# Kernel tuning notes

Hardware: AMD Instinct MI355X
Metric: run time of the kernel (lower is better)

Reference implementation:

```python
import jax, jax.numpy as jnp
import numpy as np

HID = 128  # args['hidden_size']


def preprocess_adj(A):
    # A: [B, N, N] -> D^{-1/2} (A + I) D^{-1/2}
    N = A.shape[1]
    A_hat = A + jnp.eye(N, dtype=A.dtype)
    d = jnp.sum(A_hat, axis=2)                     # [B, N]
    d_safe = jnp.where(d > 0, d, 1.0)
    d_inv = jnp.where(d > 0, d_safe ** -0.5, 0.0)  # inf -> 0, as in torch code
    return d_inv[:, :, None] * A_hat * d_inv[:, None, :]


def lstm(x, w_ih, w_hh, b_ih, b_hh):
    # x: [B, T, H]; PyTorch gate order i, f, g, o; zero init state
    B = x.shape[0]
    H = w_hh.shape[1]
    def step(carry, xt):
        h, c = carry
        z = xt @ w_ih.T + b_ih + h @ w_hh.T + b_hh
        i, f, g, o = jnp.split(z, 4, axis=-1)
        c = jax.nn.sigmoid(f) * c + jax.nn.sigmoid(i) * jnp.tanh(g)
        h = jax.nn.sigmoid(o) * jnp.tanh(c)
        return (h, c), h
    h0 = jnp.zeros((B, H), x.dtype)
    c0 = jnp.zeros((B, H), x.dtype)
    _, hs = jax.lax.scan(step, (h0, c0), jnp.swapaxes(x, 0, 1))
    return jnp.swapaxes(hs, 0, 1)  # [B, T, H]


def gcn_dynamic_forward(x, A_norm, conv_w, conv_b, w_ih, w_hh, b_ih, b_hh):
    # x: [B, N, HID] with N >= HID: take last HID rows as dynamic-filter input
    df_in = x[:, x.shape[1] - HID:, :]              # [B, HID, HID]
    dyn = jax.lax.conv_general_dilated(
        df_in, conv_w, window_strides=(1,), padding=[(1, 1)],
        dimension_numbers=('NCH', 'OIH', 'NCH')) + conv_b[None, :, None]
    lw = lstm(dyn, w_ih, w_hh, b_ih, b_hh)          # [B, HID, HID]
    agg = jnp.matmul(A_norm, x)                     # [B, N, HID]
    out = jax.nn.sigmoid(jnp.matmul(agg, lw))       # output activation (1-layer GCN)
    return out                                       # dropout is identity in eval


def setup_inputs() -> dict:
    key = jax.random.key(0)
    ks = jax.random.split(key, 8)
    B, N = 4, 4096
    node_embedding = jax.random.normal(ks[0], (B, N, HID), dtype=jnp.float32)
    # sparse symmetric-ish 0/1 adjacency, avg degree ~ N*0.01
    adjacency_matrix = (jax.random.uniform(ks[1], (B, N, N)) < 0.01).astype(jnp.float32)
    s = 0.05
    conv_w = jax.random.normal(ks[2], (HID, HID, 3), dtype=jnp.float32) * s
    conv_b = jax.random.normal(ks[3], (HID,), dtype=jnp.float32) * s
    w_ih = jax.random.normal(ks[4], (4 * HID, HID), dtype=jnp.float32) * s
    w_hh = jax.random.normal(ks[5], (4 * HID, HID), dtype=jnp.float32) * s
    b_ih = jax.random.normal(ks[6], (4 * HID,), dtype=jnp.float32) * s
    b_hh = jax.random.normal(ks[7], (4 * HID,), dtype=jnp.float32) * s
    return {"node_embedding": node_embedding, "adjacency_matrix": adjacency_matrix,
            "conv_w": conv_w, "conv_b": conv_b,
            "w_ih": w_ih, "w_hh": w_hh, "b_ih": b_ih, "b_hh": b_hh}


def reference(node_embedding, adjacency_matrix, conv_w, conv_b, w_ih, w_hh, b_ih, b_hh):
    A_norm = preprocess_adj(adjacency_matrix)
    return gcn_dynamic_forward(node_embedding, A_norm, conv_w, conv_b, w_ih, w_hh, b_ih, b_hh)
```

## Files before the change

kernel.cpp:

```cpp
#include <hip/hip_runtime.h>
#include <math.h>

#define N_NODES 4096
#define HIDN 128
#define MAXNZ 128

typedef float v4f __attribute__((ext_vector_type(4)));
typedef _Float16 h2 __attribute__((ext_vector_type(2)));
typedef _Float16 h8 __attribute__((ext_vector_type(8)));

__device__ __forceinline__ float fsig(float x) { return 1.0f / (1.0f + __expf(-x)); }
__device__ __forceinline__ float ftanh_(float x) { return 1.0f - 2.0f / (__expf(2.0f * x) + 1.0f); }

__global__ __launch_bounds__(512) void k_conv(
        const float* __restrict__ x, const float* __restrict__ conv_w,
        const float* __restrict__ conv_b, const float* __restrict__ w_ih,
        const float* __restrict__ b_ih, const float* __restrict__ b_hh,
        float* __restrict__ z4) {
    const int cb = blockIdx.x;
    const int b = cb >> 5;
    const int t0 = (cb & 31) * 4;
    const int tsub = threadIdx.x >> 7;
    const int h = threadIdx.x & 127;
    const int t = t0 + tsub;
    __shared__ __align__(16) float dyn_lds[4][HIDN];
    const float* xb = x + ((size_t)b * N_NODES + (N_NODES - HIDN)) * HIDN;
    const float* w = conv_w + (size_t)t * HIDN * 3;
    float a0 = conv_b[t], a1 = 0.0f, a2 = 0.0f, a3 = 0.0f;
    #pragma unroll 4
    for (int i = 0; i < HIDN; i += 4) {
        const float* xr0 = xb + (size_t)i * HIDN;
        #pragma unroll
        for (int s = 0; s < 4; ++s) {
            const float* xr = xr0 + s * HIDN;
            float w0 = w[(i + s) * 3 + 0], w1 = w[(i + s) * 3 + 1], w2 = w[(i + s) * 3 + 2];
            float left  = (h > 0)   ? xr[h - 1] : 0.0f;
            float mid   = xr[h];
            float right = (h < 127) ? xr[h + 1] : 0.0f;
            if (s == 0)      a0 += left * w0 + mid * w1 + right * w2;
            else if (s == 1) a1 += left * w0 + mid * w1 + right * w2;
            else if (s == 2) a2 += left * w0 + mid * w1 + right * w2;
            else             a3 += left * w0 + mid * w1 + right * w2;
        }
    }
    dyn_lds[tsub][h] = (a0 + a1) + (a2 + a3);
    __syncthreads();
    const float4* dyn4 = (const float4*)dyn_lds[tsub];
    const int ch = t >> 4, si = t & 15;
    for (int qg = 0; qg < 4; ++qg) {
        int u = h + 128 * qg;
        const float4* wr = (const float4*)(w_ih + (size_t)u * HIDN);
        float za = b_ih[u] + b_hh[u];
        #pragma unroll
        for (int f4 = 0; f4 < 32; ++f4) {
            float4 wv = wr[f4];
            float4 dv = dyn4[f4];
            za += wv.x * dv.x + wv.y * dv.y + wv.z * dv.z + wv.w * dv.w;
        }
        z4[(((size_t)(b * 8 + ch) * 128 + h) * 4 + qg) * 16 + si] = za;
    }
}

__global__ __launch_bounds__(256) void k_scan(
        const float* __restrict__ A, float* __restrict__ d_inv,
        int* __restrict__ cnt, int* __restrict__ idx) {
    const int wid = threadIdx.x >> 6;
    const int lane = threadIdx.x & 63;
    const int r = blockIdx.x * 4 + wid;
    const v4f* row = (const v4f*)(A + (size_t)r * N_NODES);
    int* idx_row = idx + r * MAXNZ;
    const unsigned long long below = (1ull << lane) - 1ull;
    int cbase = 0;
#define PROC1(c, col)                                                         \
    {                                                                         \
        bool nz = ((c) != 0.0f);                                              \
        unsigned long long mm = __ballot(nz);                                 \
        if (mm) {                                                             \
            if (nz) {                                                         \
                int p_ = cbase + __popcll(mm & below);                        \
                if (p_ < MAXNZ) idx_row[p_] = (col);                          \
            }                                                                 \
            cbase += __popcll(mm);                                            \
        }                                                                     \
    }
    for (int half = 0; half < 2; ++half) {
        v4f v[8];
        #pragma unroll
        for (int j = 0; j < 8; ++j)
            v[j] = row[half * 512 + j * 64 + lane];
        #pragma unroll
        for (int j = 0; j < 8; ++j) {
            int col0 = (half * 512 + j * 64 + lane) * 4;
            PROC1(v[j].x, col0 + 0);
            PROC1(v[j].y, col0 + 1);
            PROC1(v[j].z, col0 + 2);
            PROC1(v[j].w, col0 + 3);
        }
    }
#undef PROC1
    if (lane == 0) {
        cnt[r] = (cbase < MAXNZ) ? cbase : MAXNZ;
        d_inv[r] = rsqrtf((float)(cbase + 1));
    }
}

__global__ __launch_bounds__(512) void k_lstm(
        const float* __restrict__ z4, const float* __restrict__ w_hh,
        float* __restrict__ lw) {
    const int b = blockIdx.x;
    const int t = threadIdx.x;
    const int m = t >> 2;
    const int q = t & 3;
    __shared__ __align__(16) h2 hbuf[2][64];
    h2 w2[4][16];
    #pragma unroll
    for (int g = 0; g < 4; ++g) {
        const float4* wr = (const float4*)(w_hh + ((size_t)(g * HIDN + m)) * HIDN + q * 32);
        #pragma unroll
        for (int j4 = 0; j4 < 8; ++j4) {
            float4 wv = wr[j4];
            w2[g][2 * j4 + 0] = h2{(_Float16)wv.x, (_Float16)wv.y};
            w2[g][2 * j4 + 1] = h2{(_Float16)wv.z, (_Float16)wv.w};
        }
    }
    float c = 0.0f;
    if (t < 64) hbuf[0][t] = h2{(_Float16)0.0f, (_Float16)0.0f};
    __syncthreads();
    for (int ch = 0; ch < 8; ++ch) {
        const float4* zc = (const float4*)(z4 + ((((size_t)(b * 8 + ch) * 128 + m) * 4 + q) * 16));
        float4 zr0 = zc[0], zr1 = zc[1], zr2 = zc[2], zr3 = zc[3];
        float zs[16] = {zr0.x, zr0.y, zr0.z, zr0.w, zr1.x, zr1.y, zr1.z, zr1.w,
                        zr2.x, zr2.y, zr2.z, zr2.w, zr3.x, zr3.y, zr3.z, zr3.w};
        float hist[16];
        #pragma unroll
        for (int si = 0; si < 16; ++si) {
            const int s = ch * 16 + si;
            const h8* hq8 = ((const h8*)hbuf[s & 1]) + q * 4;
            h8 H0 = hq8[0], H1 = hq8[1], H2 = hq8[2], H3 = hq8[3];
            h2 hh[16];
            #pragma unroll
            for (int j = 0; j < 4; ++j) {
                hh[j]      = ((const h2*)&H0)[j];
                hh[4 + j]  = ((const h2*)&H1)[j];
                hh[8 + j]  = ((const h2*)&H2)[j];
                hh[12 + j] = ((const h2*)&H3)[j];
            }
            float zq = zs[si];
            float a0 = (q == 0) ? zq : 0.0f, b0 = 0.0f;
            float a1 = (q == 1) ? zq : 0.0f, b1 = 0.0f;
            float a2 = (q == 2) ? zq : 0.0f, b2 = 0.0f;
            float a3 = (q == 3) ? zq : 0.0f, b3 = 0.0f;
            #pragma unroll
            for (int j = 0; j < 8; ++j) {
                a0 = __builtin_amdgcn_fdot2(w2[0][2 * j], hh[2 * j], a0, false);
                b0 = __builtin_amdgcn_fdot2(w2[0][2 * j + 1], hh[2 * j + 1], b0, false);
                a1 = __builtin_amdgcn_fdot2(w2[1][2 * j], hh[2 * j], a1, false);
                b1 = __builtin_amdgcn_fdot2(w2[1][2 * j + 1], hh[2 * j + 1], b1, false);
                a2 = __builtin_amdgcn_fdot2(w2[2][2 * j], hh[2 * j], a2, false);
                b2 = __builtin_amdgcn_fdot2(w2[2][2 * j + 1], hh[2 * j + 1], b2, false);
                a3 = __builtin_amdgcn_fdot2(w2[3][2 * j], hh[2 * j], a3, false);
                b3 = __builtin_amdgcn_fdot2(w2[3][2 * j + 1], hh[2 * j + 1], b3, false);
            }
            float z0 = a0 + b0, z1 = a1 + b1, z2 = a2 + b2, z3 = a3 + b3;
            z0 += __shfl_xor(z0, 1); z0 += __shfl_xor(z0, 2);
            z1 += __shfl_xor(z1, 1); z1 += __shfl_xor(z1, 2);
            z2 += __shfl_xor(z2, 1); z2 += __shfl_xor(z2, 2);
            z3 += __shfl_xor(z3, 1); z3 += __shfl_xor(z3, 2);
            float ig = fsig(z0);
            float fg = fsig(z1);
            float gg = ftanh_(z2);
            float og = fsig(z3);
            c = fg * c + ig * gg;
            float hn = og * ftanh_(c);
            hist[si] = hn;
            if (q == 0) ((_Float16*)hbuf[(s + 1) & 1])[m] = (_Float16)hn;
            __syncthreads();
        }
        float* lwb = lw + ((size_t)b * HIDN + ch * 16) * HIDN + m;
        #pragma unroll
        for (int qq = 0; qq < 4; ++qq) {
            if (q == qq) {
                #pragma unroll
                for (int k = 0; k < 4; ++k)
                    lwb[(size_t)(qq * 4 + k) * HIDN] = hist[qq * 4 + k];
            }
        }
    }
}

__global__ __launch_bounds__(256) void k_gather(
        const float* __restrict__ x, const float* __restrict__ d_inv,
        const int* __restrict__ cnt, const int* __restrict__ idx,
        float* __restrict__ agg) {
    const int bIdx = blockIdx.x;
    const int b = (bIdx & 7) >> 1;
    const int o = ((bIdx >> 3) << 1) | (bIdx & 1);
    const int wid = threadIdx.x >> 6;
    const int lane = threadIdx.x & 63;
    __shared__ __align__(16) float dl[N_NODES];
    {
        const float4* dsrc = (const float4*)(d_inv + (b << 12));
        float4* ddst = (float4*)dl;
        #pragma unroll
        for (int k = 0; k < 4; ++k)
            ddst[threadIdx.x + 256 * k] = dsrc[threadIdx.x + 256 * k];
    }
    __syncthreads();
    const int i = o * 4 + wid;
    const int r = (b << 12) + i;
    const float2* xb = (const float2*)(x + (size_t)b * N_NODES * HIDN);
    const int* irow = idx + r * MAXNZ;
    const int n = cnt[r];
    float ax = 0.0f, ay = 0.0f;
    int k = 0;
    for (; k + 8 <= n; k += 8) {
        int4 j0 = *(const int4*)&irow[k];
        int4 j1 = *(const int4*)&irow[k + 4];
        float2 v0 = xb[(size_t)j0.x * 64 + lane];
        float2 v1 = xb[(size_t)j0.y * 64 + lane];
        float2 v2 = xb[(size_t)j0.z * 64 + lane];
        float2 v3 = xb[(size_t)j0.w * 64 + lane];
        float2 v4 = xb[(size_t)j1.x * 64 + lane];
        float2 v5 = xb[(size_t)j1.y * 64 + lane];
        float2 v6 = xb[(size_t)j1.z * 64 + lane];
        float2 v7 = xb[(size_t)j1.w * 64 + lane];
        float d0 = dl[j0.x], d1 = dl[j0.y], d2 = dl[j0.z], d3 = dl[j0.w];
        float d4 = dl[j1.x], d5 = dl[j1.y], d6 = dl[j1.z], d7 = dl[j1.w];
        ax += d0 * v0.x + d1 * v1.x + d2 * v2.x + d3 * v3.x
            + d4 * v4.x + d5 * v5.x + d6 * v6.x + d7 * v7.x;
        ay += d0 * v0.y + d1 * v1.y + d2 * v2.y + d3 * v3.y
            + d4 * v4.y + d5 * v5.y + d6 * v6.y + d7 * v7.y;
    }
    for (; k < n; ++k) {
        int j = irow[k];
        float dj = dl[j];
        float2 v = xb[(size_t)j * 64 + lane];
        ax += dj * v.x;
        ay += dj * v.y;
    }
    float di = dl[i];
    float2 vi = xb[(size_t)i * 64 + lane];
    float2 out;
    out.x = di * (ax + di * vi.x);
    out.y = di * (ay + di * vi.y);
    ((float2*)(agg + (size_t)r * HIDN))[lane] = out;
}

__global__ __launch_bounds__(256) void k_outmm(
        const float* __restrict__ agg, const float* __restrict__ lw,
        float* __restrict__ out) {
    __shared__ __align__(16) float lw_lds[HIDN * HIDN];
    const int i0 = blockIdx.x * 64;
    const int b = i0 >> 12;
    const float4* lwg = (const float4*)(lw + (size_t)b * HIDN * HIDN);
    float4* lds4 = (float4*)lw_lds;
    for (int v = threadIdx.x; v < HIDN * HIDN / 4; v += 256) lds4[v] = lwg[v];
    __syncthreads();
    const int r0 = i0 + (threadIdx.x >> 3) * 2;
    const int u0 = (threadIdx.x & 7) * 16;
    const float4* a4 = (const float4*)agg;
    float4 acc[2][4];
    #pragma unroll
    for (int rr = 0; rr < 2; ++rr)
        #pragma unroll
        for (int cc = 0; cc < 4; ++cc) acc[rr][cc] = make_float4(0.f, 0.f, 0.f, 0.f);
    for (int f4 = 0; f4 < 32; ++f4) {
        float4 a0 = a4[(size_t)r0 * 32 + f4];
        float4 a1 = a4[(size_t)(r0 + 1) * 32 + f4];
        #pragma unroll
        for (int ff = 0; ff < 4; ++ff) {
            float af0 = (ff == 0) ? a0.x : (ff == 1) ? a0.y : (ff == 2) ? a0.z : a0.w;
            float af1 = (ff == 0) ? a1.x : (ff == 1) ? a1.y : (ff == 2) ? a1.z : a1.w;
            int f = f4 * 4 + ff;
            const float4* wrow = (const float4*)(lw_lds + f * HIDN + u0);
            #pragma unroll
            for (int cc = 0; cc < 4; ++cc) {
                float4 wv = wrow[cc];
                acc[0][cc].x += af0 * wv.x; acc[0][cc].y += af0 * wv.y;
                acc[0][cc].z += af0 * wv.z; acc[0][cc].w += af0 * wv.w;
                acc[1][cc].x += af1 * wv.x; acc[1][cc].y += af1 * wv.y;
                acc[1][cc].z += af1 * wv.z; acc[1][cc].w += af1 * wv.w;
            }
        }
    }
    #pragma unroll
    for (int rr = 0; rr < 2; ++rr) {
        #pragma unroll
        for (int cc = 0; cc < 4; ++cc) {
            float4 ov;
            ov.x = fsig(acc[rr][cc].x);
            ov.y = fsig(acc[rr][cc].y);
            ov.z = fsig(acc[rr][cc].z);
            ov.w = fsig(acc[rr][cc].w);
            *(float4*)(out + (size_t)(r0 + rr) * HIDN + u0 + cc * 4) = ov;
        }
    }
}

extern "C" void kernel_launch(void* const* d_in, const int* in_sizes, int n_in,
                              void* d_out, int out_size, void* d_ws, size_t ws_size,
                              hipStream_t stream) {
    const float* x      = (const float*)d_in[0];
    const float* A      = (const float*)d_in[1];
    const float* conv_w = (const float*)d_in[2];
    const float* conv_b = (const float*)d_in[3];
    const float* w_ih   = (const float*)d_in[4];
    const float* w_hh   = (const float*)d_in[5];
    const float* b_ih   = (const float*)d_in[6];
    const float* b_hh   = (const float*)d_in[7];
    float* out = (float*)d_out;

    char* ws = (char*)d_ws;
    float* d_inv = (float*)ws;
    int*   cnt   = (int*)(ws + 65536);
    int*   idx   = (int*)(ws + 131072);
    float* z4    = (float*)(ws + 131072 + 8388608);
    float* lw    = (float*)(ws + 131072 + 8388608 + 1048576);
    float* agg   = (float*)(ws + 131072 + 8388608 + 1048576 + 262144);

    hipLaunchKernelGGL(k_conv, dim3(128), dim3(512), 0, stream,
                       x, conv_w, conv_b, w_ih, b_ih, b_hh, z4);
    hipLaunchKernelGGL(k_scan, dim3(4096), dim3(256), 0, stream,
                       A, d_inv, cnt, idx);
    hipLaunchKernelGGL(k_lstm, dim3(4), dim3(512), 0, stream, z4, w_hh, lw);
    hipLaunchKernelGGL(k_gather, dim3(4096), dim3(256), 0, stream,
                       x, d_inv, cnt, idx, agg);
    hipLaunchKernelGGL(k_outmm, dim3(256), dim3(256), 0, stream, agg, lw, out);
}
```

Measured before the change: 606.9 us.

## Merge independent kernels into combined launches so conv/scan and LSTM/gather overlap

Combines the adjacency scan and the conv/input-projection kernel into one launch, with blocks split by blockIdx. It likewise combines the sequential LSTM (4 blocks) and the neighbor gather into one launch, and switches both to 512-thread blocks. The aim is to hide the long serial LSTM behind the bandwidth-heavy gather and cut launch count, with nontemporal loads for the one-pass adjacency read. In exchange, the merged kernels share register and LDS budgets, which may lower occupancy for the gather and scan parts.

```diff
diff --git a/kernel.cpp b/kernel.cpp
--- a/kernel.cpp
+++ b/kernel.cpp
@@ -12,238 +12,237 @@
 __device__ __forceinline__ float fsig(float x) { return 1.0f / (1.0f + __expf(-x)); }
 __device__ __forceinline__ float ftanh_(float x) { return 1.0f - 2.0f / (__expf(2.0f * x) + 1.0f); }
 
-__global__ __launch_bounds__(512) void k_conv(
+__global__ __launch_bounds__(512) void k_scan_conv(
+        const float* __restrict__ A, float* __restrict__ d_inv,
+        int* __restrict__ cnt, int* __restrict__ idx,
         const float* __restrict__ x, const float* __restrict__ conv_w,
         const float* __restrict__ conv_b, const float* __restrict__ w_ih,
         const float* __restrict__ b_ih, const float* __restrict__ b_hh,
         float* __restrict__ z4) {
-    const int cb = blockIdx.x;
-    const int b = cb >> 5;
-    const int t0 = (cb & 31) * 4;
-    const int tsub = threadIdx.x >> 7;
-    const int h = threadIdx.x & 127;
-    const int t = t0 + tsub;
-    __shared__ __align__(16) float dyn_lds[4][HIDN];
-    const float* xb = x + ((size_t)b * N_NODES + (N_NODES - HIDN)) * HIDN;
-    const float* w = conv_w + (size_t)t * HIDN * 3;
-    float a0 = conv_b[t], a1 = 0.0f, a2 = 0.0f, a3 = 0.0f;
-    #pragma unroll 4
-    for (int i = 0; i < HIDN; i += 4) {
-        const float* xr0 = xb + (size_t)i * HIDN;
-        #pragma unroll
-        for (int s = 0; s < 4; ++s) {
-            const float* xr = xr0 + s * HIDN;
-            float w0 = w[(i + s) * 3 + 0], w1 = w[(i + s) * 3 + 1], w2 = w[(i + s) * 3 + 2];
-            float left  = (h > 0)   ? xr[h - 1] : 0.0f;
-            float mid   = xr[h];
-            float right = (h < 127) ? xr[h + 1] : 0.0f;
-            if (s == 0)      a0 += left * w0 + mid * w1 + right * w2;
-            else if (s == 1) a1 += left * w0 + mid * w1 + right * w2;
-            else if (s == 2) a2 += left * w0 + mid * w1 + right * w2;
-            else             a3 += left * w0 + mid * w1 + right * w2;
-        }
-    }
-    dyn_lds[tsub][h] = (a0 + a1) + (a2 + a3);
-    __syncthreads();
-    const float4* dyn4 = (const float4*)dyn_lds[tsub];
-    const int ch = t >> 4, si = t & 15;
-    for (int qg = 0; qg < 4; ++qg) {
-        int u = h + 128 * qg;
-        const float4* wr = (const float4*)(w_ih + (size_t)u * HIDN);
-        float za = b_ih[u] + b_hh[u];
-        #pragma unroll
-        for (int f4 = 0; f4 < 32; ++f4) {
-            float4 wv = wr[f4];
-            float4 dv = dyn4[f4];
-            za += wv.x * dv.x + wv.y * dv.y + wv.z * dv.z + wv.w * dv.w;
-        }
-        z4[(((size_t)(b * 8 + ch) * 128 + h) * 4 + qg) * 16 + si] = za;
+    if (blockIdx.x < 2048) {
+        const int wid = threadIdx.x >> 6;
+        const int lane = threadIdx.x & 63;
+        const int r = blockIdx.x * 8 + wid;
+        const v4f* row = (const v4f*)(A + (size_t)r * N_NODES);
+        int* idx_row = idx + r * MAXNZ;
+        const unsigned long long below = (1ull << lane) - 1ull;
+        int cbase = 0;
+#define PROC1(c, col)                                                         \
+        {                                                                     \
+            bool nz = ((c) != 0.0f);                                          \
+            unsigned long long mm = __ballot(nz);                             \
+            if (mm) {                                                         \
+                if (nz) {                                                     \
+                    int p_ = cbase + __popcll(mm & below);                    \
+                    if (p_ < MAXNZ) idx_row[p_] = (col);                      \
+                }                                                             \
+                cbase += __popcll(mm);                                        \
+            }                                                                 \
+        }
+        for (int half = 0; half < 2; ++half) {
+            v4f v[8];
+            #pragma unroll
+            for (int j = 0; j < 8; ++j)
+                v[j] = __builtin_nontemporal_load(&row[half * 512 + j * 64 + lane]);
+            #pragma unroll
+            for (int j = 0; j < 8; ++j) {
+                int col0 = (half * 512 + j * 64 + lane) * 4;
+                PROC1(v[j].x, col0 + 0);
+                PROC1(v[j].y, col0 + 1);
+                PROC1(v[j].z, col0 + 2);
+                PROC1(v[j].w, col0 + 3);
+            }
+        }
+#undef PROC1
+        if (lane == 0) {
+            cnt[r] = (cbase < MAXNZ) ? cbase : MAXNZ;
+            d_inv[r] = rsqrtf((float)(cbase + 1));
+        }
+    } else {
+        const int cb = blockIdx.x - 2048;
+        const int b = cb >> 5;
+        const int t0 = (cb & 31) * 4;
+        const int tsub = threadIdx.x >> 7;
+        const int h = threadIdx.x & 127;
+        const int t = t0 + tsub;
+        __shared__ __align__(16) float dyn_lds[4][HIDN];
+        const float* xb = x + ((size_t)b * N_NODES + (N_NODES - HIDN)) * HIDN;
+        const float* w = conv_w + (size_t)t * HIDN * 3;
+        float a0 = conv_b[t], a1 = 0.0f, a2 = 0.0f, a3 = 0.0f;
+        #pragma unroll 4
+        for (int i = 0; i < HIDN; i += 4) {
+            const float* xr0 = xb + (size_t)i * HIDN;
+            #pragma unroll
+            for (int s = 0; s < 4; ++s) {
+                const float* xr = xr0 + s * HIDN;
+                float w0 = w[(i + s) * 3 + 0], w1 = w[(i + s) * 3 + 1], w2 = w[(i + s) * 3 + 2];
+                float left  = (h > 0)   ? xr[h - 1] : 0.0f;
+                float mid   = xr[h];
+                float right = (h < 127) ? xr[h + 1] : 0.0f;
+                if (s == 0)      a0 += left * w0 + mid * w1 + right * w2;
+                else if (s == 1) a1 += left * w0 + mid * w1 + right * w2;
+                else if (s == 2) a2 += left * w0 + mid * w1 + right * w2;
+                else             a3 += left * w0 + mid * w1 + right * w2;
+            }
+        }
+        dyn_lds[tsub][h] = (a0 + a1) + (a2 + a3);
+        __syncthreads();
+        const float4* dyn4 = (const float4*)dyn_lds[tsub];
+        const int ch = t >> 4, si = t & 15;
+        for (int qg = 0; qg < 4; ++qg) {
+            int u = h + 128 * qg;
+            const float4* wr = (const float4*)(w_ih + (size_t)u * HIDN);
+            float za = b_ih[u] + b_hh[u];
+            #pragma unroll
+            for (int f4 = 0; f4 < 32; ++f4) {
+                float4 wv = wr[f4];
+                float4 dv = dyn4[f4];
+                za += wv.x * dv.x + wv.y * dv.y + wv.z * dv.z + wv.w * dv.w;
+            }
+            z4[(((size_t)(b * 8 + ch) * 128 + h) * 4 + qg) * 16 + si] = za;
+        }
     }
 }
 
-__global__ __launch_bounds__(256) void k_scan(
-        const float* __restrict__ A, float* __restrict__ d_inv,
-        int* __restrict__ cnt, int* __restrict__ idx) {
-    const int wid = threadIdx.x >> 6;
-    const int lane = threadIdx.x & 63;
-    const int r = blockIdx.x * 4 + wid;
-    const v4f* row = (const v4f*)(A + (size_t)r * N_NODES);
-    int* idx_row = idx + r * MAXNZ;
-    const unsigned long long below = (1ull << lane) - 1ull;
-    int cbase = 0;
-#define PROC1(c, col)                                                         \
-    {                                                                         \
-        bool nz = ((c) != 0.0f);                                              \
-        unsigned long long mm = __ballot(nz);                                 \
-        if (mm) {                                                             \
-            if (nz) {                                                         \
-                int p_ = cbase + __popcll(mm & below);                        \
-                if (p_ < MAXNZ) idx_row[p_] = (col);                          \
-            }                                                                 \
-            cbase += __popcll(mm);                                            \
-        }                                                                     \
-    }
-    for (int half = 0; half < 2; ++half) {
-        v4f v[8];
-        #pragma unroll
-        for (int j = 0; j < 8; ++j)
-            v[j] = row[half * 512 + j * 64 + lane];
-        #pragma unroll
-        for (int j = 0; j < 8; ++j) {
-            int col0 = (half * 512 + j * 64 + lane) * 4;
-            PROC1(v[j].x, col0 + 0);
-            PROC1(v[j].y, col0 + 1);
-            PROC1(v[j].z, col0 + 2);
-            PROC1(v[j].w, col0 + 3);
-        }
-    }
-#undef PROC1
-    if (lane == 0) {
-        cnt[r] = (cbase < MAXNZ) ? cbase : MAXNZ;
-        d_inv[r] = rsqrtf((float)(cbase + 1));
-    }
-}
-
-__global__ __launch_bounds__(512) void k_lstm(
+__global__ __launch_bounds__(512) void k_lstm_gather(
         const float* __restrict__ z4, const float* __restrict__ w_hh,
-        float* __restrict__ lw) {
-    const int b = blockIdx.x;
-    const int t = threadIdx.x;
-    const int m = t >> 2;
-    const int q = t & 3;
-    __shared__ __align__(16) h2 hbuf[2][64];
-    h2 w2[4][16];
-    #pragma unroll
-    for (int g = 0; g < 4; ++g) {
-        const float4* wr = (const float4*)(w_hh + ((size_t)(g * HIDN + m)) * HIDN + q * 32);
-        #pragma unroll
-        for (int j4 = 0; j4 < 8; ++j4) {
-            float4 wv = wr[j4];
-            w2[g][2 * j4 + 0] = h2{(_Float16)wv.x, (_Float16)wv.y};
-            w2[g][2 * j4 + 1] = h2{(_Float16)wv.z, (_Float16)wv.w};
-        }
-    }
-    float c = 0.0f;
-    if (t < 64) hbuf[0][t] = h2{(_Float16)0.0f, (_Float16)0.0f};
-    __syncthreads();
-    for (int ch = 0; ch < 8; ++ch) {
-        const float4* zc = (const float4*)(z4 + ((((size_t)(b * 8 + ch) * 128 + m) * 4 + q) * 16));
-        float4 zr0 = zc[0], zr1 = zc[1], zr2 = zc[2], zr3 = zc[3];
-        float zs[16] = {zr0.x, zr0.y, zr0.z, zr0.w, zr1.x, zr1.y, zr1.z, zr1.w,
-                        zr2.x, zr2.y, zr2.z, zr2.w, zr3.x, zr3.y, zr3.z, zr3.w};
-        float hist[16];
-        #pragma unroll
-        for (int si = 0; si < 16; ++si) {
-            const int s = ch * 16 + si;
-            const h8* hq8 = ((const h8*)hbuf[s & 1]) + q * 4;
-            h8 H0 = hq8[0], H1 = hq8[1], H2 = hq8[2], H3 = hq8[3];
-            h2 hh[16];
-            #pragma unroll
-            for (int j = 0; j < 4; ++j) {
-                hh[j]      = ((const h2*)&H0)[j];
-                hh[4 + j]  = ((const h2*)&H1)[j];
-                hh[8 + j]  = ((const h2*)&H2)[j];
-                hh[12 + j] = ((const h2*)&H3)[j];
-            }
-            float zq = zs[si];
-            float a0 = (q == 0) ? zq : 0.0f, b0 = 0.0f;
-            float a1 = (q == 1) ? zq : 0.0f, b1 = 0.0f;
-            float a2 = (q == 2) ? zq : 0.0f, b2 = 0.0f;
-            float a3 = (q == 3) ? zq : 0.0f, b3 = 0.0f;
-            #pragma unroll
-            for (int j = 0; j < 8; ++j) {
-                a0 = __builtin_amdgcn_fdot2(w2[0][2 * j], hh[2 * j], a0, false);
-                b0 = __builtin_amdgcn_fdot2(w2[0][2 * j + 1], hh[2 * j + 1], b0, false);
-                a1 = __builtin_amdgcn_fdot2(w2[1][2 * j], hh[2 * j], a1, false);
-                b1 = __builtin_amdgcn_fdot2(w2[1][2 * j + 1], hh[2 * j + 1], b1, false);
-                a2 = __builtin_amdgcn_fdot2(w2[2][2 * j], hh[2 * j], a2, false);
-                b2 = __builtin_amdgcn_fdot2(w2[2][2 * j + 1], hh[2 * j + 1], b2, false);
-                a3 = __builtin_amdgcn_fdot2(w2[3][2 * j], hh[2 * j], a3, false);
-                b3 = __builtin_amdgcn_fdot2(w2[3][2 * j + 1], hh[2 * j + 1], b3, false);
-            }
-            float z0 = a0 + b0, z1 = a1 + b1, z2 = a2 + b2, z3 = a3 + b3;
-            z0 += __shfl_xor(z0, 1); z0 += __shfl_xor(z0, 2);
-            z1 += __shfl_xor(z1, 1); z1 += __shfl_xor(z1, 2);
-            z2 += __shfl_xor(z2, 1); z2 += __shfl_xor(z2, 2);
-            z3 += __shfl_xor(z3, 1); z3 += __shfl_xor(z3, 2);
-            float ig = fsig(z0);
-            float fg = fsig(z1);
-            float gg = ftanh_(z2);
-            float og = fsig(z3);
-            c = fg * c + ig * gg;
-            float hn = og * ftanh_(c);
-            hist[si] = hn;
-            if (q == 0) ((_Float16*)hbuf[(s + 1) & 1])[m] = (_Float16)hn;
-            __syncthreads();
-        }
-        float* lwb = lw + ((size_t)b * HIDN + ch * 16) * HIDN + m;
-        #pragma unroll
-        for (int qq = 0; qq < 4; ++qq) {
-            if (q == qq) {
-                #pragma unroll
-                for (int k = 0; k < 4; ++k)
-                    lwb[(size_t)(qq * 4 + k) * HIDN] = hist[qq * 4 + k];
-            }
-        }
-    }
-}
-
-__global__ __launch_bounds__(256) void k_gather(
+        float* __restrict__ lw,
         const float* __restrict__ x, const float* __restrict__ d_inv,
         const int* __restrict__ cnt, const int* __restrict__ idx,
         float* __restrict__ agg) {
-    const int bIdx = blockIdx.x;
-    const int b = (bIdx & 7) >> 1;
-    const int o = ((bIdx >> 3) << 1) | (bIdx & 1);
-    const int wid = threadIdx.x >> 6;
-    const int lane = threadIdx.x & 63;
-    __shared__ __align__(16) float dl[N_NODES];
-    {
-        const float4* dsrc = (const float4*)(d_inv + (b << 12));
-        float4* ddst = (float4*)dl;
+    if (blockIdx.x < 4) {
+        const int b = blockIdx.x;
+        const int t = threadIdx.x;
+        const int m = t >> 2;
+        const int q = t & 3;
+        __shared__ __align__(16) h2 hbuf[2][64];
+        h2 w2[4][16];
         #pragma unroll
-        for (int k = 0; k < 4; ++k)
-            ddst[threadIdx.x + 256 * k] = dsrc[threadIdx.x + 256 * k];
+        for (int g = 0; g < 4; ++g) {
+            const float4* wr = (const float4*)(w_hh + ((size_t)(g * HIDN + m)) * HIDN + q * 32);
+            #pragma unroll
+            for (int j4 = 0; j4 < 8; ++j4) {
+                float4 wv = wr[j4];
+                w2[g][2 * j4 + 0] = h2{(_Float16)wv.x, (_Float16)wv.y};
+                w2[g][2 * j4 + 1] = h2{(_Float16)wv.z, (_Float16)wv.w};
+            }
+        }
+        float c = 0.0f;
+        if (t < 64) hbuf[0][t] = h2{(_Float16)0.0f, (_Float16)0.0f};
+        __syncthreads();
+        for (int ch = 0; ch < 8; ++ch) {
+            const float4* zc = (const float4*)(z4 + ((((size_t)(b * 8 + ch) * 128 + m) * 4 + q) * 16));
+            float4 zr0 = zc[0], zr1 = zc[1], zr2 = zc[2], zr3 = zc[3];
+            float zs[16] = {zr0.x, zr0.y, zr0.z, zr0.w, zr1.x, zr1.y, zr1.z, zr1.w,
+                            zr2.x, zr2.y, zr2.z, zr2.w, zr3.x, zr3.y, zr3.z, zr3.w};
+            float hist[16];
+            #pragma unroll
+            for (int si = 0; si < 16; ++si) {
+                const int s = ch * 16 + si;
+                const h8* hq8 = ((const h8*)hbuf[s & 1]) + q * 4;
+                h8 H0 = hq8[0], H1 = hq8[1], H2 = hq8[2], H3 = hq8[3];
+                h2 hh[16];
+                #pragma unroll
+                for (int j = 0; j < 4; ++j) {
+                    hh[j]      = ((const h2*)&H0)[j];
+                    hh[4 + j]  = ((const h2*)&H1)[j];
+                    hh[8 + j]  = ((const h2*)&H2)[j];
+                    hh[12 + j] = ((const h2*)&H3)[j];
+                }
+                float zq = zs[si];
+                float a0 = (q == 0) ? zq : 0.0f, b0 = 0.0f;
+                float a1 = (q == 1) ? zq : 0.0f, b1 = 0.0f;
+                float a2 = (q == 2) ? zq : 0.0f, b2 = 0.0f;
+                float a3 = (q == 3) ? zq : 0.0f, b3 = 0.0f;
+                #pragma unroll
+                for (int j = 0; j < 8; ++j) {
+                    a0 = __builtin_amdgcn_fdot2(w2[0][2 * j], hh[2 * j], a0, false);
+                    b0 = __builtin_amdgcn_fdot2(w2[0][2 * j + 1], hh[2 * j + 1], b0, false);
+                    a1 = __builtin_amdgcn_fdot2(w2[1][2 * j], hh[2 * j], a1, false);
+                    b1 = __builtin_amdgcn_fdot2(w2[1][2 * j + 1], hh[2 * j + 1], b1, false);
+                    a2 = __builtin_amdgcn_fdot2(w2[2][2 * j], hh[2 * j], a2, false);
+                    b2 = __builtin_amdgcn_fdot2(w2[2][2 * j + 1], hh[2 * j + 1], b2, false);
+                    a3 = __builtin_amdgcn_fdot2(w2[3][2 * j], hh[2 * j], a3, false);
+                    b3 = __builtin_amdgcn_fdot2(w2[3][2 * j + 1], hh[2 * j + 1], b3, false);
+                }
+                float z0 = a0 + b0, z1 = a1 + b1, z2 = a2 + b2, z3 = a3 + b3;
+                z0 += __shfl_xor(z0, 1); z0 += __shfl_xor(z0, 2);
+                z1 += __shfl_xor(z1, 1); z1 += __shfl_xor(z1, 2);
+                z2 += __shfl_xor(z2, 1); z2 += __shfl_xor(z2, 2);
+                z3 += __shfl_xor(z3, 1); z3 += __shfl_xor(z3, 2);
+                float ig = fsig(z0);
+                float fg = fsig(z1);
+                float gg = ftanh_(z2);
+                float og = fsig(z3);
+                c = fg * c + ig * gg;
+                float hn = og * ftanh_(c);
+                hist[si] = hn;
+                if (q == 0) ((_Float16*)hbuf[(s + 1) & 1])[m] = (_Float16)hn;
+                __syncthreads();
+            }
+            float* lwb = lw + ((size_t)b * HIDN + ch * 16) * HIDN + m;
+            #pragma unroll
+            for (int qq = 0; qq < 4; ++qq) {
+                if (q == qq) {
+                    #pragma unroll
+                    for (int k = 0; k < 4; ++k)
+                        lwb[(size_t)(qq * 4 + k) * HIDN] = hist[qq * 4 + k];
+                }
+            }
+        }
+    } else {
+        const int gIdx = blockIdx.x - 4;
+        const int b = (gIdx & 7) >> 1;
+        const int o = ((gIdx >> 3) << 1) | (gIdx & 1);
+        const int wid = threadIdx.x >> 6;
+        const int lane = threadIdx.x & 63;
+        __shared__ __align__(16) float dl[N_NODES];
+        {
+            const float4* dsrc = (const float4*)(d_inv + (b << 12));
+            float4* ddst = (float4*)dl;
+            ddst[threadIdx.x] = dsrc[threadIdx.x];
+            ddst[threadIdx.x + 512] = dsrc[threadIdx.x + 512];
+        }
+        __syncthreads();
+        const int i = o * 8 + wid;
+        const int r = (b << 12) + i;
+        const float2* xb = (const float2*)(x + (size_t)b * N_NODES * HIDN);
+        const int* irow = idx + r * MAXNZ;
+        const int n = cnt[r];
+        float ax = 0.0f, ay = 0.0f;
+        int k = 0;
+        for (; k + 8 <= n; k += 8) {
+            int4 j0 = *(const int4*)&irow[k];
+            int4 j1 = *(const int4*)&irow[k + 4];
+            float2 v0 = xb[(size_t)j0.x * 64 + lane];
+            float2 v1 = xb[(size_t)j0.y * 64 + lane];
+            float2 v2 = xb[(size_t)j0.z * 64 + lane];
+            float2 v3 = xb[(size_t)j0.w * 64 + lane];
+            float2 v4 = xb[(size_t)j1.x * 64 + lane];
+            float2 v5 = xb[(size_t)j1.y * 64 + lane];
+            float2 v6 = xb[(size_t)j1.z * 64 + lane];
+            float2 v7 = xb[(size_t)j1.w * 64 + lane];
+            float d0 = dl[j0.x], d1 = dl[j0.y], d2 = dl[j0.z], d3 = dl[j0.w];
+            float d4 = dl[j1.x], d5 = dl[j1.y], d6 = dl[j1.z], d7 = dl[j1.w];
+            ax += d0 * v0.x + d1 * v1.x + d2 * v2.x + d3 * v3.x
+                + d4 * v4.x + d5 * v5.x + d6 * v6.x + d7 * v7.x;
+            ay += d0 * v0.y + d1 * v1.y + d2 * v2.y + d3 * v3.y
+                + d4 * v4.y + d5 * v5.y + d6 * v6.y + d7 * v7.y;
+        }
+        for (; k < n; ++k) {
+            int j = irow[k];
+            float dj = dl[j];
+            float2 v = xb[(size_t)j * 64 + lane];
+            ax += dj * v.x;
+            ay += dj * v.y;
+        }
+        float di = dl[i];
+        float2 vi = xb[(size_t)i * 64 + lane];
+        float2 o2;
+        o2.x = di * (ax + di * vi.x);
+        o2.y = di * (ay + di * vi.y);
+        ((float2*)(agg + (size_t)r * HIDN))[lane] = o2;
     }
-    __syncthreads();
-    const int i = o * 4 + wid;
-    const int r = (b << 12) + i;
-    const float2* xb = (const float2*)(x + (size_t)b * N_NODES * HIDN);
-    const int* irow = idx + r * MAXNZ;
-    const int n = cnt[r];
-    float ax = 0.0f, ay = 0.0f;
-    int k = 0;
-    for (; k + 8 <= n; k += 8) {
-        int4 j0 = *(const int4*)&irow[k];
-        int4 j1 = *(const int4*)&irow[k + 4];
-        float2 v0 = xb[(size_t)j0.x * 64 + lane];
-        float2 v1 = xb[(size_t)j0.y * 64 + lane];
-        float2 v2 = xb[(size_t)j0.z * 64 + lane];
-        float2 v3 = xb[(size_t)j0.w * 64 + lane];
-        float2 v4 = xb[(size_t)j1.x * 64 + lane];
-        float2 v5 = xb[(size_t)j1.y * 64 + lane];
-        float2 v6 = xb[(size_t)j1.z * 64 + lane];
-        float2 v7 = xb[(size_t)j1.w * 64 + lane];
-        float d0 = dl[j0.x], d1 = dl[j0.y], d2 = dl[j0.z], d3 = dl[j0.w];
-        float d4 = dl[j1.x], d5 = dl[j1.y], d6 = dl[j1.z], d7 = dl[j1.w];
-        ax += d0 * v0.x + d1 * v1.x + d2 * v2.x + d3 * v3.x
-            + d4 * v4.x + d5 * v5.x + d6 * v6.x + d7 * v7.x;
-        ay += d0 * v0.y + d1 * v1.y + d2 * v2.y + d3 * v3.y
-            + d4 * v4.y + d5 * v5.y + d6 * v6.y + d7 * v7.y;
-    }
-    for (; k < n; ++k) {
-        int j = irow[k];
-        float dj = dl[j];
-        float2 v = xb[(size_t)j * 64 + lane];
-        ax += dj * v.x;
-        ay += dj * v.y;
-    }
-    float di = dl[i];
-    float2 vi = xb[(size_t)i * 64 + lane];
-    float2 out;
-    out.x = di * (ax + di * vi.x);
-    out.y = di * (ay + di * vi.y);
-    ((float2*)(agg + (size_t)r * HIDN))[lane] = out;
 }
 
 __global__ __launch_bounds__(256) void k_outmm(
@@ -318,12 +317,10 @@
     float* lw    = (float*)(ws + 131072 + 8388608 + 1048576);
     float* agg   = (float*)(ws + 131072 + 8388608 + 1048576 + 262144);
 
-    hipLaunchKernelGGL(k_conv, dim3(128), dim3(512), 0, stream,
+    hipLaunchKernelGGL(k_scan_conv, dim3(2176), dim3(512), 0, stream,
+                       A, d_inv, cnt, idx,
                        x, conv_w, conv_b, w_ih, b_ih, b_hh, z4);
-    hipLaunchKernelGGL(k_scan, dim3(4096), dim3(256), 0, stream,
-                       A, d_inv, cnt, idx);
-    hipLaunchKernelGGL(k_lstm, dim3(4), dim3(512), 0, stream, z4, w_hh, lw);
-    hipLaunchKernelGGL(k_gather, dim3(4096), dim3(256), 0, stream,
-                       x, d_inv, cnt, idx, agg);
+    hipLaunchKernelGGL(k_lstm_gather, dim3(2052), dim3(512), 0, stream,
+                       z4, w_hh, lw, x, d_inv, cnt, idx, agg);
     hipLaunchKernelGGL(k_outmm, dim3(256), dim3(256), 0, stream, agg, lw, out);
 }
```

After: 553.3 us. 1.1x faster.
